# Kernel tuning notes

Measured on AMD Instinct MI355X. Metric: run time of the kernel, lower is better.

The kernel has to match this reference:

```python
import jax, jax.numpy as jnp
import numpy as np

B, C, W, H = 4, 256, 64, 64


def setup_inputs() -> dict:
    key = jax.random.key(0)
    ks = jax.random.split(key, 10)
    s = 1.0 / np.sqrt(C)  # fan-in style scale for 1x1 conv weights
    return {
        "x": jax.random.normal(ks[0], (B, C, W, H), dtype=jnp.float32),
        "Wq": jax.random.normal(ks[1], (C, C), dtype=jnp.float32) * s,
        "bq": jax.random.normal(ks[2], (C,), dtype=jnp.float32) * 0.02,
        "Wk": jax.random.normal(ks[3], (C, C), dtype=jnp.float32) * s,
        "bk": jax.random.normal(ks[4], (C,), dtype=jnp.float32) * 0.02,
        "Wv": jax.random.normal(ks[5], (C, C), dtype=jnp.float32) * s,
        "bv": jax.random.normal(ks[6], (C,), dtype=jnp.float32) * 0.02,
        "rel_h": jax.random.normal(ks[7], (1, C, H, 1), dtype=jnp.float32),
        "rel_w": jax.random.normal(ks[8], (1, C, 1, W), dtype=jnp.float32),
        # gamma is initialized to 0 in the original; use a nonzero value so the
        # attention branch actually contributes (otherwise out == x).
        "gamma": jnp.full((1,), 0.5, dtype=jnp.float32),
    }


def reference(x, Wq, bq, Wk, bk, Wv, bv, rel_h, rel_w, gamma):
    Bz, Cc, Ww, Hh = x.shape
    N = Ww * Hh
    xf = x.reshape(Bz, Cc, N)  # [B, C, N]

    # 1x1 convs == per-pixel linear projections over channels
    q = jnp.einsum('oc,bcn->bno', Wq, xf) + bq            # [B, N, C]
    k = jnp.einsum('oc,bcn->bon', Wk, xf) + bk[:, None]   # [B, C, N]
    v = jnp.einsum('oc,bcn->bon', Wv, xf) + bv[:, None]   # [B, C, N]

    # relative position bias: (rel_h + rel_w) -> [C, N], projected by q
    pos = (rel_h + rel_w).reshape(Cc, N)                  # [C, N]
    energy = jnp.einsum('bnc,bcm->bnm', q, k) + q @ pos   # [B, N, N]

    att = jax.nn.softmax(energy, axis=-1)                 # [B, N, N]

    # out[b,c,m] = sum_n v[b,c,n] * att[b,m,n]
    out = jnp.einsum('bcn,bmn->bcm', v, att).reshape(Bz, Cc, Ww, Hh)
    return gamma * out + x
```

## Files before the change

### kernel.cpp

```cpp
#include <hip/hip_runtime.h>
#include <stdint.h>

#define N_TOK 4096
#define C_DIM 256

typedef __attribute__((ext_vector_type(8))) short short8;
typedef __attribute__((ext_vector_type(8))) _Float16 half8;
typedef __attribute__((ext_vector_type(4))) float floatx4;
typedef __attribute__((ext_vector_type(4))) unsigned short ushort4v;

__device__ __forceinline__ unsigned short bf16_rne(float f) {
    union { float f; unsigned int u; } v; v.f = f;
    unsigned int u = v.u;
    unsigned int rounded = u + 0x7FFFu + ((u >> 16) & 1u);
    return (unsigned short)(rounded >> 16);
}
__device__ __forceinline__ float bf16_to_f(unsigned short h) {
    union { unsigned int u; float f; } v; v.u = ((unsigned int)h) << 16;
    return v.f;
}
__device__ __forceinline__ void split_bf16(float f, unsigned short& h, unsigned short& l) {
    h = bf16_rne(f);
    l = bf16_rne(f - bf16_to_f(h));
}
__device__ __forceinline__ unsigned short f2h(float f) {
    union { _Float16 h; unsigned short u; } v; v.h = (_Float16)f; return v.u;
}
__device__ __forceinline__ float h2f(unsigned short u) {
    union { unsigned short u; _Float16 h; } v; v.u = u; return (float)v.h;
}
__device__ __forceinline__ unsigned int pack2h(float a, float b) {
    union { _Float16 h[2]; unsigned int u; } v;
    v.h[0] = (_Float16)a; v.h[1] = (_Float16)b;
    return v.u;
}
__device__ __forceinline__ void g2l16(const void* g, void* l) {
    __builtin_amdgcn_global_load_lds(
        (const __attribute__((address_space(1))) void*)g,
        (__attribute__((address_space(3))) void*)l, 16, 0, 0);
}

__global__ __launch_bounds__(256) void prep_kernel(
    const float* __restrict__ x,
    const float* __restrict__ Wq, const float* __restrict__ Wk, const float* __restrict__ Wv,
    unsigned short* __restrict__ Xhi, unsigned short* __restrict__ Xlo,
    unsigned short* __restrict__ Whi, unsigned short* __restrict__ Wlo)
{
    const int t = threadIdx.x;
    if (blockIdx.x >= 1024) {
        const int pj = blockIdx.x - 1024;
        const float* W = (pj == 0) ? Wq : (pj == 1) ? Wk : Wv;
        unsigned short* dh = Whi + pj * 65536;
        unsigned short* dl = Wlo + pj * 65536;
        for (int it = 0; it < 64; it++) {
            const int idx = it * 1024 + t * 4;
            const float4 w = *(const float4*)&W[idx];
            unsigned short h0, l0, h1, l1, h2, l2, h3, l3;
            split_bf16(w.x, h0, l0); split_bf16(w.y, h1, l1);
            split_bf16(w.z, h2, l2); split_bf16(w.w, h3, l3);
            ushort4v vh; vh[0] = h0; vh[1] = h1; vh[2] = h2; vh[3] = h3;
            ushort4v vl; vl[0] = l0; vl[1] = l1; vl[2] = l2; vl[3] = l3;
            *(ushort4v*)&dh[idx] = vh;
            *(ushort4v*)&dl[idx] = vl;
        }
        return;
    }
    __shared__ float Xs[64 * 65];
    const int b  = blockIdx.x >> 8;
    const int ct = (blockIdx.x >> 6) & 3;
    const int nt = blockIdx.x & 63;
    const int c0 = ct * 64, n0 = nt * 64;
    {
        const int nch = t & 15, cr = t >> 4;
#pragma unroll
        for (int pass = 0; pass < 4; pass++) {
            const int c = pass * 16 + cr;
            const float4 v = *(const float4*)&x[((size_t)(b * C_DIM + c0 + c)) * N_TOK + n0 + nch * 4];
            float* row = &Xs[c * 65 + nch * 4];
            row[0] = v.x; row[1] = v.y; row[2] = v.z; row[3] = v.w;
        }
    }
    __syncthreads();
    {
        const int n = t >> 2, cc = t & 3;
        short8 vh0, vl0, vh1, vl1;
#pragma unroll
        for (int i = 0; i < 8; i++) {
            unsigned short h, l;
            split_bf16(Xs[(cc * 16 + i) * 65 + n], h, l);
            vh0[i] = (short)h; vl0[i] = (short)l;
        }
#pragma unroll
        for (int i = 0; i < 8; i++) {
            unsigned short h, l;
            split_bf16(Xs[(cc * 16 + 8 + i) * 65 + n], h, l);
            vh1[i] = (short)h; vl1[i] = (short)l;
        }
        const size_t off = ((size_t)b * N_TOK + n0 + n) * C_DIM + c0 + cc * 16;
        *(short8*)&Xhi[off] = vh0; *(short8*)&Xhi[off + 8] = vh1;
        *(short8*)&Xlo[off] = vl0; *(short8*)&Xlo[off + 8] = vl1;
    }
}

__global__ __launch_bounds__(256) void proj_kernel(
    const unsigned short* __restrict__ Xhi, const unsigned short* __restrict__ Xlo,
    const unsigned short* __restrict__ Whi, const unsigned short* __restrict__ Wlo,
    const float* __restrict__ bq, const float* __restrict__ bk, const float* __restrict__ bv,
    const float* __restrict__ relh, const float* __restrict__ relw,
    unsigned short* __restrict__ Qh,
    unsigned short* __restrict__ Kh,
    unsigned short* __restrict__ Vh)
{
    __shared__ unsigned short SM[20480];
    unsigned short* Ah = SM;
    unsigned short* Al = SM + 2048;
    unsigned short* Bh = SM + 4096;
    unsigned short* Bl = SM + 12288;

    const int t    = threadIdx.x;
    const int wave = t >> 6;
    const int lane = t & 63;
    const int l15  = lane & 15;
    const int quad = lane >> 4;

    const int bp   = blockIdx.x >> 6;
    const int proj = bp % 3;
    const int b    = bp / 3;
    const int n0   = (blockIdx.x & 63) * 64;

    const unsigned short* Xh = Xhi + ((size_t)b * N_TOK + n0) * C_DIM;
    const unsigned short* Xl = Xlo + ((size_t)b * N_TOK + n0) * C_DIM;
    const unsigned short* Wh = Whi + proj * 65536;
    const unsigned short* Wl = Wlo + proj * 65536;
    const float* bias = (proj == 0) ? bq : (proj == 1) ? bk : bv;
    const bool needlo = (proj < 2);

    floatx4 acc[16];
#pragma unroll
    for (int i = 0; i < 16; i++) acc[i] = (floatx4){0.f, 0.f, 0.f, 0.f};

    for (int c0 = 0; c0 < 256; c0 += 32) {
        {
            const int lr = lane >> 2, cp = lane & 3;
            const int key = (lr ^ (lr >> 2)) & 3;
            const int r = wave * 16 + lr;
            g2l16(Xh + (size_t)r * C_DIM + c0 + (cp ^ key) * 8, &Ah[wave * 512]);
            if (needlo) g2l16(Xl + (size_t)r * C_DIM + c0 + (cp ^ key) * 8, &Al[wave * 512]);
#pragma unroll
            for (int p = 0; p < 4; p++) {
                const int rb = (p * 4 + wave) * 16;
                const int rr = rb + lr;
                g2l16(Wh + (size_t)rr * 256 + c0 + (cp ^ key) * 8, &Bh[rb * 32]);
                if (needlo) g2l16(Wl + (size_t)rr * 256 + c0 + (cp ^ key) * 8, &Bl[rb * 32]);
            }
        }
        __syncthreads();

        const int akey = (l15 ^ (l15 >> 2)) & 3;
        const int arow = (wave * 16 + l15) * 32 + ((quad ^ akey) * 8);
        const short8 a_h = *(const short8*)&Ah[arow];
        short8 a_l;
        if (needlo) a_l = *(const short8*)&Al[arow];
#pragma unroll
        for (int ot = 0; ot < 16; ot++) {
            const int brow = (ot * 16 + l15) * 32 + ((quad ^ akey) * 8);
            const short8 b_h = *(const short8*)&Bh[brow];
            acc[ot] = __builtin_amdgcn_mfma_f32_16x16x32_bf16(a_h, b_h, acc[ot], 0, 0, 0);
            if (needlo) {
                const short8 b_l = *(const short8*)&Bl[brow];
                acc[ot] = __builtin_amdgcn_mfma_f32_16x16x32_bf16(a_l, b_h, acc[ot], 0, 0, 0);
                acc[ot] = __builtin_amdgcn_mfma_f32_16x16x32_bf16(a_h, b_l, acc[ot], 0, 0, 0);
            }
        }
        __syncthreads();
    }

    const int h0 = n0 >> 6;
    if (proj == 0) {
        unsigned short* Og = Qh + ((size_t)b * N_TOK + n0) * C_DIM;
#pragma unroll
        for (int ot = 0; ot < 16; ot++) {
            const int o = ot * 16 + l15;
            const float bs = bias[o];
#pragma unroll
            for (int r = 0; r < 4; r++) {
                const int nl = wave * 16 + quad * 4 + r;
                Og[(size_t)nl * C_DIM + o] = f2h(acc[ot][r] + bs);
            }
        }
    } else if (proj == 1) {
        unsigned short* Og = Kh + ((size_t)b * N_TOK + n0) * C_DIM;
#pragma unroll
        for (int ot = 0; ot < 16; ot++) {
            const int o = ot * 16 + l15;
            const float bs = bias[o];
            const float ph = relh[o * 64 + h0];
#pragma unroll
            for (int r = 0; r < 4; r++) {
                const int nl = wave * 16 + quad * 4 + r;
                Og[(size_t)nl * C_DIM + o] = f2h(acc[ot][r] + bs + ph + relw[o * 64 + nl]);
            }
        }
    } else {
        unsigned short* Vt = SM;
#pragma unroll
        for (int ot = 0; ot < 16; ot++) {
            const int o = ot * 16 + l15;
            const float bs = bias[o];
            const unsigned int u0 = (unsigned int)f2h(acc[ot][0] + bs) |
                                    ((unsigned int)f2h(acc[ot][1] + bs) << 16);
            const unsigned int u1 = (unsigned int)f2h(acc[ot][2] + bs) |
                                    ((unsigned int)f2h(acc[ot][3] + bs) << 16);
            uint2 uv; uv.x = u0; uv.y = u1;
            *(uint2*)&Vt[o * 72 + wave * 16 + quad * 4] = uv;
        }
        __syncthreads();
        const int ch   = t & 7;
        const int orow = t >> 3;
#pragma unroll
        for (int pass = 0; pass < 8; pass++) {
            const int o = pass * 32 + orow;
            const short8 vv = *(const short8*)&Vt[o * 72 + ch * 8];
            *(short8*)&Vh[((size_t)b * C_DIM + o) * N_TOK + n0 + ch * 8] = vv;
        }
    }
}

__global__ __launch_bounds__(256, 2) void flash_kernel(
    const unsigned short* __restrict__ Qg,
    const unsigned short* __restrict__ Kg,
    const unsigned short* __restrict__ Vg,
    unsigned short* __restrict__ Op,
    float* __restrict__ Lm)
{
    constexpr int NITER = 32;

    __shared__ unsigned short Ks[64 * 256];
    __shared__ unsigned short Vs[256 * 64];

    const int t    = threadIdx.x;
    const int wave = t >> 6;
    const int lane = t & 63;
    const int l15  = lane & 15;
    const int quad = lane >> 4;
    const int lk   = l15 & 7;

    const int bid = blockIdx.x;
    const int b   = bid & 3;
    const int s   = (bid >> 2) & 1;
    const int qt  = bid >> 3;

    const unsigned short* Kb = Kg + (size_t)b * N_TOK * C_DIM;
    const unsigned short* Vb = Vg + (size_t)b * C_DIM * N_TOK;

    half8 qf[8];
    const int qrow = qt * 64 + wave * 16 + l15;
    {
        const unsigned short* Qrow = Qg + ((size_t)b * N_TOK + qrow) * C_DIM;
#pragma unroll
        for (int ct = 0; ct < 8; ct++)
            qf[ct] = *(const half8*)&Qrow[ct * 32 + quad * 8];
    }

    floatx4 oacc[16];
#pragma unroll
    for (int i = 0; i < 16; i++) oacc[i] = (floatx4){0.f, 0.f, 0.f, 0.f};
    float m_i = -1e30f;
    float l_i = 0.f;

    const int jbase = s * (NITER * 64);
    const int oddq  = quad & 1;
    const int hiq   = quad >> 1;
    const int own   = (quad == 0) | (quad == 3);

    {
        const int lr = lane >> 5, cp = lane & 31;
#pragma unroll
        for (int p = 0; p < 8; p++) {
            const int jl = wave * 16 + p * 2 + lr;
            g2l16(Kb + (size_t)(jbase + jl) * C_DIM + (cp ^ (jl & 7)) * 8,
                  &Ks[(wave * 16 + p * 2) * 256]);
        }
    }

    for (int ti = 0; ti < NITER; ti++) {
        const int j0 = jbase + ti * 64;

        __syncthreads();

        {
            const int lr = lane >> 3, cp = lane & 7;
#pragma unroll
            for (int p = 0; p < 8; p++) {
                const int ob = (p * 4 + wave) * 8;
                const int o  = ob + lr;
                g2l16(Vb + (size_t)o * N_TOK + j0 + (cp ^ (o & 7)) * 8, &Vs[ob * 64]);
            }
        }

        floatx4 sv[4];
        __builtin_amdgcn_s_setprio(1);
#pragma unroll
        for (int jt = 0; jt < 4; jt++) {
            floatx4 a = (floatx4){0.f, 0.f, 0.f, 0.f};
#pragma unroll
            for (int ct = 0; ct < 8; ct++) {
                const half8 kb = *(const half8*)&Ks[(jt * 16 + l15) * 256 + (((ct * 4 + quad) ^ lk) * 8)];
                a = __builtin_amdgcn_mfma_f32_16x16x32_f16(kb, qf[ct], a, 0, 0, 0);
            }
            sv[jt] = a;
        }
        __builtin_amdgcn_s_setprio(0);

        float mx;
        {
            const float a0 = fmaxf(fmaxf(sv[0][0], sv[0][1]), fmaxf(sv[0][2], sv[0][3]));
            const float a1 = fmaxf(fmaxf(sv[1][0], sv[1][1]), fmaxf(sv[1][2], sv[1][3]));
            const float a2 = fmaxf(fmaxf(sv[2][0], sv[2][1]), fmaxf(sv[2][2], sv[2][3]));
            const float a3 = fmaxf(fmaxf(sv[3][0], sv[3][1]), fmaxf(sv[3][2], sv[3][3]));
            mx = fmaxf(fmaxf(a0, a1), fmaxf(a2, a3));
        }
        mx = fmaxf(mx, __shfl_xor(mx, 16));
        mx = fmaxf(mx, __shfl_xor(mx, 32));

        if (!__all(mx <= m_i + 8.f)) {
            const float mn    = fmaxf(m_i, mx);
            const float alpha = __expf(m_i - mn);
            m_i = mn;
            l_i *= alpha;
#pragma unroll
            for (int ot = 0; ot < 16; ot++) {
                oacc[ot][0] *= alpha; oacc[ot][1] *= alpha;
                oacc[ot][2] *= alpha; oacc[ot][3] *= alpha;
            }
        }
        float ps = 0.f;
#pragma unroll
        for (int jt = 0; jt < 4; jt++) {
#pragma unroll
            for (int r = 0; r < 4; r++) {
                const float p = __expf(sv[jt][r] - m_i);
                sv[jt][r] = p;
                ps += p;
            }
        }
        l_i += ps;

        half8 pf0, pf1;
        {
            const unsigned int u00 = pack2h(sv[0][0], sv[0][1]);
            const unsigned int u01 = pack2h(sv[0][2], sv[0][3]);
            const unsigned int u10 = pack2h(sv[1][0], sv[1][1]);
            const unsigned int u11 = pack2h(sv[1][2], sv[1][3]);
            const unsigned int t00 = __shfl_xor(u00, 16), t01 = __shfl_xor(u01, 16);
            const unsigned int t10 = __shfl_xor(u10, 16), t11 = __shfl_xor(u11, 16);
            const unsigned int L00 = oddq ? t00 : u00, H00 = oddq ? u00 : t00;
            const unsigned int L01 = oddq ? t01 : u01, H01 = oddq ? u01 : t01;
            const unsigned int L10 = oddq ? t10 : u10, H10 = oddq ? u10 : t10;
            const unsigned int L11 = oddq ? t11 : u11, H11 = oddq ? u11 : t11;
            const unsigned int ke0 = hiq ? L10 : L00, se0 = hiq ? L00 : L10;
            const unsigned int ke1 = hiq ? L11 : L01, se1 = hiq ? L01 : L11;
            const unsigned int ko0 = hiq ? H10 : H00, so0 = hiq ? H00 : H10;
            const unsigned int ko1 = hiq ? H11 : H01, so1 = hiq ? H01 : H11;
            const unsigned int re0 = __shfl_xor(se0, 32), re1 = __shfl_xor(se1, 32);
            const unsigned int ro0 = __shfl_xor(so0, 32), ro1 = __shfl_xor(so1, 32);
            union { unsigned int u[4]; half8 h; } pk;
            pk.u[0] = own ? ke0 : re0;
            pk.u[1] = own ? ke1 : re1;
            pk.u[2] = own ? ko0 : ro0;
            pk.u[3] = own ? ko1 : ro1;
            pf0 = pk.h;
        }
        {
            const unsigned int u00 = pack2h(sv[2][0], sv[2][1]);
            const unsigned int u01 = pack2h(sv[2][2], sv[2][3]);
            const unsigned int u10 = pack2h(sv[3][0], sv[3][1]);
            const unsigned int u11 = pack2h(sv[3][2], sv[3][3]);
            const unsigned int t00 = __shfl_xor(u00, 16), t01 = __shfl_xor(u01, 16);
            const unsigned int t10 = __shfl_xor(u10, 16), t11 = __shfl_xor(u11, 16);
            const unsigned int L00 = oddq ? t00 : u00, H00 = oddq ? u00 : t00;
            const unsigned int L01 = oddq ? t01 : u01, H01 = oddq ? u01 : t01;
            const unsigned int L10 = oddq ? t10 : u10, H10 = oddq ? u10 : t10;
            const unsigned int L11 = oddq ? t11 : u11, H11 = oddq ? u11 : t11;
            const unsigned int ke0 = hiq ? L10 : L00, se0 = hiq ? L00 : L10;
            const unsigned int ke1 = hiq ? L11 : L01, se1 = hiq ? L01 : L11;
            const unsigned int ko0 = hiq ? H10 : H00, so0 = hiq ? H00 : H10;
            const unsigned int ko1 = hiq ? H11 : H01, so1 = hiq ? H01 : H11;
            const unsigned int re0 = __shfl_xor(se0, 32), re1 = __shfl_xor(se1, 32);
            const unsigned int ro0 = __shfl_xor(so0, 32), ro1 = __shfl_xor(so1, 32);
            union { unsigned int u[4]; half8 h; } pk;
            pk.u[0] = own ? ke0 : re0;
            pk.u[1] = own ? ke1 : re1;
            pk.u[2] = own ? ko0 : ro0;
            pk.u[3] = own ? ko1 : ro1;
            pf1 = pk.h;
        }

        __syncthreads();

        if (ti < NITER - 1) {
            const int lr = lane >> 5, cp = lane & 31;
#pragma unroll
            for (int p = 0; p < 8; p++) {
                const int jl = wave * 16 + p * 2 + lr;
                g2l16(Kb + (size_t)(j0 + 64 + jl) * C_DIM + (cp ^ (jl & 7)) * 8,
                      &Ks[(wave * 16 + p * 2) * 256]);
            }
        }

        __builtin_amdgcn_s_setprio(1);
#pragma unroll
        for (int ot = 0; ot < 16; ot++) {
            const int row = (ot * 16 + l15) * 64;
            const half8 av0 = *(const half8*)&Vs[row + ((quad ^ lk) * 8)];
            const half8 av1 = *(const half8*)&Vs[row + (((4 + quad) ^ lk) * 8)];
            oacc[ot] = __builtin_amdgcn_mfma_f32_16x16x32_f16(av0, pf0, oacc[ot], 0, 0, 0);
            oacc[ot] = __builtin_amdgcn_mfma_f32_16x16x32_f16(av1, pf1, oacc[ot], 0, 0, 0);
        }
        __builtin_amdgcn_s_setprio(0);
    }

    unsigned short* Ob = Op + ((size_t)(s * 4 + b) * C_DIM) * N_TOK;
    const int n = qt * 64 + wave * 16 + l15;
#pragma unroll
    for (int ot = 0; ot < 16; ot++) {
#pragma unroll
        for (int r = 0; r < 4; r++) {
            const int c = ot * 16 + quad * 4 + r;
            Ob[(size_t)c * N_TOK + n] = f2h(oacc[ot][r]);
        }
    }
    float lt = l_i;
    lt += __shfl_xor(lt, 16);
    lt += __shfl_xor(lt, 32);
    if (quad == 0) {
        const size_t nb = (size_t)(s * 4 + b) * N_TOK + n;
        *(float2*)&Lm[nb * 2] = make_float2(m_i, lt);
    }
}

__global__ __launch_bounds__(256) void merge_kernel(
    const unsigned short* __restrict__ Op,
    const float* __restrict__ Lm,
    const float* __restrict__ x,
    const float* __restrict__ gamma,
    float* __restrict__ out)
{
    constexpr int NS = 2;
    const int blk = blockIdx.x;
    const int b   = blk >> 10;
    const int c   = (blk >> 2) & 255;
    const int nq  = blk & 3;
    const int n0  = nq * 1024 + threadIdx.x * 4;

    const size_t NEo = (size_t)4 * C_DIM * N_TOK;
    const size_t obase = ((size_t)b * C_DIM + c) * N_TOK + n0;

    float ms[NS][4], ls[NS][4], os[NS][4];
#pragma unroll
    for (int s = 0; s < NS; s++) {
        const uint2 u = *(const uint2*)&Op[s * NEo + obase];
        os[s][0] = h2f((unsigned short)(u.x & 0xffff));
        os[s][1] = h2f((unsigned short)(u.x >> 16));
        os[s][2] = h2f((unsigned short)(u.y & 0xffff));
        os[s][3] = h2f((unsigned short)(u.y >> 16));
        const float* Lms = Lm + (size_t)(s * 4 + b) * N_TOK * 2;
        const float4 A0 = *(const float4*)&Lms[n0 * 2];
        const float4 A1 = *(const float4*)&Lms[n0 * 2 + 4];
        ms[s][0] = A0.x; ls[s][0] = A0.y;
        ms[s][1] = A0.z; ls[s][1] = A0.w;
        ms[s][2] = A1.x; ls[s][2] = A1.y;
        ms[s][3] = A1.z; ls[s][3] = A1.w;
    }
    const float4 xv = *(const float4*)&x[obase];
    const float xin[4] = {xv.x, xv.y, xv.z, xv.w};
    const float g = gamma[0];

    float4 res;
    float* rp = (float*)&res;
#pragma unroll
    for (int i = 0; i < 4; i++) {
        float M = ms[0][i];
#pragma unroll
        for (int s = 1; s < NS; s++) M = fmaxf(M, ms[s][i]);
        float osum = 0.f, lsum = 0.f;
#pragma unroll
        for (int s = 0; s < NS; s++) {
            const float w = __expf(ms[s][i] - M);
            osum += w * os[s][i];
            lsum += w * ls[s][i];
        }
        rp[i] = g * osum / lsum + xin[i];
    }
    *(float4*)&out[obase] = res;
}

extern "C" void kernel_launch(void* const* d_in, const int* in_sizes, int n_in,
                              void* d_out, int out_size, void* d_ws, size_t ws_size,
                              hipStream_t stream) {
    const float* x     = (const float*)d_in[0];
    const float* Wq    = (const float*)d_in[1];
    const float* bq    = (const float*)d_in[2];
    const float* Wk    = (const float*)d_in[3];
    const float* bk    = (const float*)d_in[4];
    const float* Wv    = (const float*)d_in[5];
    const float* bv    = (const float*)d_in[6];
    const float* relh  = (const float*)d_in[7];
    const float* relw  = (const float*)d_in[8];
    const float* gamma = (const float*)d_in[9];
    float* out = (float*)d_out;

    const size_t NE = (size_t)4 * N_TOK * C_DIM;

    unsigned short* Op  = (unsigned short*)d_ws;
    unsigned short* Xhi = Op;
    unsigned short* Xlo = Op + NE;
    unsigned short* Whi = Op + (size_t)2 * NE;
    unsigned short* Wlo = Whi + 3 * 65536;
    unsigned short* Qh  = Wlo + 3 * 65536;
    unsigned short* Kh  = Qh + NE;
    unsigned short* Vh  = Kh + NE;
    float* Lm = (float*)(Vh + NE);

    hipLaunchKernelGGL(prep_kernel, dim3(1027), dim3(256), 0, stream,
                       x, Wq, Wk, Wv, Xhi, Xlo, Whi, Wlo);
    hipLaunchKernelGGL(proj_kernel, dim3(768), dim3(256), 0, stream,
                       Xhi, Xlo, Whi, Wlo, bq, bk, bv, relh, relw, Qh, Kh, Vh);
    hipLaunchKernelGGL(flash_kernel, dim3(512), dim3(256), 0, stream,
                       Qh, Kh, Vh, Op, Lm);
    hipLaunchKernelGGL(merge_kernel, dim3(4096), dim3(256), 0, stream,
                       Op, Lm, x, gamma, out);
}
```

Measured before the change: 249.6 us.

## Switch flash kernel to 32x32 MFMA tiles and 4-way KV split

Rewrites the attention kernel to use 32x32x16 MFMA instructions, so each wave owns 32 query rows instead of 16 and each block covers 128 queries. This cuts LDS fragment reads per FLOP and removes the complex cross-quad shuffle repacking of P. When the workspace is large enough, the KV range is split four ways (16 iterations per block) to keep 512 blocks in flight, and merge combines 4 partials. The cost is more accumulator registers (128 floats of oacc), which may pressure occupancy at 2 blocks/CU, plus extra partial-output traffic in the merge.

```diff
diff --git a/kernel.cpp b/kernel.cpp
--- a/kernel.cpp
+++ b/kernel.cpp
@@ -7,6 +7,7 @@
 typedef __attribute__((ext_vector_type(8))) short short8;
 typedef __attribute__((ext_vector_type(8))) _Float16 half8;
 typedef __attribute__((ext_vector_type(4))) float floatx4;
+typedef __attribute__((ext_vector_type(16))) float floatx16;
 typedef __attribute__((ext_vector_type(4))) unsigned short ushort4v;
 
 __device__ __forceinline__ unsigned short bf16_rne(float f) {
@@ -226,6 +227,7 @@
     }
 }
 
+template<int NITER>
 __global__ __launch_bounds__(256, 2) void flash_kernel(
     const unsigned short* __restrict__ Qg,
     const unsigned short* __restrict__ Kg,
@@ -233,7 +235,8 @@
     unsigned short* __restrict__ Op,
     float* __restrict__ Lm)
 {
-    constexpr int NITER = 32;
+    constexpr int NS  = N_TOK / (NITER * 64);
+    constexpr int QSH = (NS == 4) ? 4 : 3;
 
     __shared__ unsigned short Ks[64 * 256];
     __shared__ unsigned short Vs[256 * 64];
@@ -241,37 +244,36 @@
     const int t    = threadIdx.x;
     const int wave = t >> 6;
     const int lane = t & 63;
-    const int l15  = lane & 15;
-    const int quad = lane >> 4;
-    const int lk   = l15 & 7;
+    const int l31  = lane & 31;
+    const int H    = lane >> 5;
+    const int lk7  = lane & 7;
 
     const int bid = blockIdx.x;
     const int b   = bid & 3;
-    const int s   = (bid >> 2) & 1;
-    const int qt  = bid >> 3;
+    const int s   = (bid >> 2) & (NS - 1);
+    const int qt  = bid >> QSH;
 
     const unsigned short* Kb = Kg + (size_t)b * N_TOK * C_DIM;
     const unsigned short* Vb = Vg + (size_t)b * C_DIM * N_TOK;
 
-    half8 qf[8];
-    const int qrow = qt * 64 + wave * 16 + l15;
+    half8 qf[16];
+    const int q0 = qt * 128 + wave * 32;
     {
-        const unsigned short* Qrow = Qg + ((size_t)b * N_TOK + qrow) * C_DIM;
-#pragma unroll
-        for (int ct = 0; ct < 8; ct++)
-            qf[ct] = *(const half8*)&Qrow[ct * 32 + quad * 8];
-    }
-
-    floatx4 oacc[16];
-#pragma unroll
-    for (int i = 0; i < 16; i++) oacc[i] = (floatx4){0.f, 0.f, 0.f, 0.f};
+        const unsigned short* Qrow = Qg + ((size_t)b * N_TOK + q0 + l31) * C_DIM + H * 8;
+#pragma unroll
+        for (int ct = 0; ct < 16; ct++)
+            qf[ct] = *(const half8*)&Qrow[ct * 16];
+    }
+
+    floatx16 oacc[8];
+#pragma unroll
+    for (int cb = 0; cb < 8; cb++)
+#pragma unroll
+        for (int r = 0; r < 16; r++) oacc[cb][r] = 0.f;
     float m_i = -1e30f;
     float l_i = 0.f;
 
     const int jbase = s * (NITER * 64);
-    const int oddq  = quad & 1;
-    const int hiq   = quad >> 1;
-    const int own   = (quad == 0) | (quad == 3);
 
     {
         const int lr = lane >> 5, cp = lane & 31;
@@ -298,29 +300,31 @@
             }
         }
 
-        floatx4 sv[4];
-        __builtin_amdgcn_s_setprio(1);
-#pragma unroll
-        for (int jt = 0; jt < 4; jt++) {
-            floatx4 a = (floatx4){0.f, 0.f, 0.f, 0.f};
-#pragma unroll
-            for (int ct = 0; ct < 8; ct++) {
-                const half8 kb = *(const half8*)&Ks[(jt * 16 + l15) * 256 + (((ct * 4 + quad) ^ lk) * 8)];
-                a = __builtin_amdgcn_mfma_f32_16x16x32_f16(kb, qf[ct], a, 0, 0, 0);
-            }
-            sv[jt] = a;
-        }
-        __builtin_amdgcn_s_setprio(0);
-
-        float mx;
+        floatx16 sv0, sv1;
         {
-            const float a0 = fmaxf(fmaxf(sv[0][0], sv[0][1]), fmaxf(sv[0][2], sv[0][3]));
-            const float a1 = fmaxf(fmaxf(sv[1][0], sv[1][1]), fmaxf(sv[1][2], sv[1][3]));
-            const float a2 = fmaxf(fmaxf(sv[2][0], sv[2][1]), fmaxf(sv[2][2], sv[2][3]));
-            const float a3 = fmaxf(fmaxf(sv[3][0], sv[3][1]), fmaxf(sv[3][2], sv[3][3]));
-            mx = fmaxf(fmaxf(a0, a1), fmaxf(a2, a3));
-        }
-        mx = fmaxf(mx, __shfl_xor(mx, 16));
+            floatx16 a0, a1;
+#pragma unroll
+            for (int r = 0; r < 16; r++) { a0[r] = 0.f; a1[r] = 0.f; }
+            const int rb0 = l31 * 256;
+            const int rb1 = (32 + l31) * 256;
+            __builtin_amdgcn_s_setprio(1);
+#pragma unroll
+            for (int ct = 0; ct < 16; ct++) {
+                const int ch = ((ct * 2 + H) ^ lk7) * 8;
+                const half8 k0 = *(const half8*)&Ks[rb0 + ch];
+                a0 = __builtin_amdgcn_mfma_f32_32x32x16_f16(k0, qf[ct], a0, 0, 0, 0);
+                const half8 k1 = *(const half8*)&Ks[rb1 + ch];
+                a1 = __builtin_amdgcn_mfma_f32_32x32x16_f16(k1, qf[ct], a1, 0, 0, 0);
+            }
+            __builtin_amdgcn_s_setprio(0);
+            sv0 = a0; sv1 = a1;
+        }
+
+        float mx = sv0[0];
+#pragma unroll
+        for (int r = 1; r < 16; r++) mx = fmaxf(mx, sv0[r]);
+#pragma unroll
+        for (int r = 0; r < 16; r++) mx = fmaxf(mx, sv1[r]);
         mx = fmaxf(mx, __shfl_xor(mx, 32));
 
         if (!__all(mx <= m_i + 8.f)) {
@@ -329,71 +333,71 @@
             m_i = mn;
             l_i *= alpha;
 #pragma unroll
-            for (int ot = 0; ot < 16; ot++) {
-                oacc[ot][0] *= alpha; oacc[ot][1] *= alpha;
-                oacc[ot][2] *= alpha; oacc[ot][3] *= alpha;
-            }
+            for (int cb = 0; cb < 8; cb++)
+#pragma unroll
+                for (int r = 0; r < 16; r++) oacc[cb][r] *= alpha;
         }
         float ps = 0.f;
 #pragma unroll
-        for (int jt = 0; jt < 4; jt++) {
-#pragma unroll
-            for (int r = 0; r < 4; r++) {
-                const float p = __expf(sv[jt][r] - m_i);
-                sv[jt][r] = p;
-                ps += p;
-            }
+        for (int r = 0; r < 16; r++) {
+            const float p = __expf(sv0[r] - m_i);
+            sv0[r] = p; ps += p;
+        }
+#pragma unroll
+        for (int r = 0; r < 16; r++) {
+            const float p = __expf(sv1[r] - m_i);
+            sv1[r] = p; ps += p;
         }
         l_i += ps;
 
-        half8 pf0, pf1;
+        half8 pf0, pf1, pf2, pf3;
         {
-            const unsigned int u00 = pack2h(sv[0][0], sv[0][1]);
-            const unsigned int u01 = pack2h(sv[0][2], sv[0][3]);
-            const unsigned int u10 = pack2h(sv[1][0], sv[1][1]);
-            const unsigned int u11 = pack2h(sv[1][2], sv[1][3]);
-            const unsigned int t00 = __shfl_xor(u00, 16), t01 = __shfl_xor(u01, 16);
-            const unsigned int t10 = __shfl_xor(u10, 16), t11 = __shfl_xor(u11, 16);
-            const unsigned int L00 = oddq ? t00 : u00, H00 = oddq ? u00 : t00;
-            const unsigned int L01 = oddq ? t01 : u01, H01 = oddq ? u01 : t01;
-            const unsigned int L10 = oddq ? t10 : u10, H10 = oddq ? u10 : t10;
-            const unsigned int L11 = oddq ? t11 : u11, H11 = oddq ? u11 : t11;
-            const unsigned int ke0 = hiq ? L10 : L00, se0 = hiq ? L00 : L10;
-            const unsigned int ke1 = hiq ? L11 : L01, se1 = hiq ? L01 : L11;
-            const unsigned int ko0 = hiq ? H10 : H00, so0 = hiq ? H00 : H10;
-            const unsigned int ko1 = hiq ? H11 : H01, so1 = hiq ? H01 : H11;
-            const unsigned int re0 = __shfl_xor(se0, 32), re1 = __shfl_xor(se1, 32);
-            const unsigned int ro0 = __shfl_xor(so0, 32), ro1 = __shfl_xor(so1, 32);
-            union { unsigned int u[4]; half8 h; } pk;
-            pk.u[0] = own ? ke0 : re0;
-            pk.u[1] = own ? ke1 : re1;
-            pk.u[2] = own ? ko0 : ro0;
-            pk.u[3] = own ? ko1 : ro1;
-            pf0 = pk.h;
+            const unsigned int p0 = pack2h(sv0[0],  sv0[1]);
+            const unsigned int p1 = pack2h(sv0[2],  sv0[3]);
+            const unsigned int p2 = pack2h(sv0[4],  sv0[5]);
+            const unsigned int p3 = pack2h(sv0[6],  sv0[7]);
+            const unsigned int p4 = pack2h(sv0[8],  sv0[9]);
+            const unsigned int p5 = pack2h(sv0[10], sv0[11]);
+            const unsigned int p6 = pack2h(sv0[12], sv0[13]);
+            const unsigned int p7 = pack2h(sv0[14], sv0[15]);
+            const unsigned int s0 = __shfl_xor(p0, 32);
+            const unsigned int s1 = __shfl_xor(p1, 32);
+            const unsigned int s2 = __shfl_xor(p2, 32);
+            const unsigned int s3 = __shfl_xor(p3, 32);
+            const unsigned int s4 = __shfl_xor(p4, 32);
+            const unsigned int s5 = __shfl_xor(p5, 32);
+            const unsigned int s6 = __shfl_xor(p6, 32);
+            const unsigned int s7 = __shfl_xor(p7, 32);
+            union { unsigned int u[4]; half8 h; } a, c;
+            a.u[0] = H ? s2 : p0;  a.u[1] = H ? s3 : p1;
+            a.u[2] = H ? p2 : s0;  a.u[3] = H ? p3 : s1;
+            c.u[0] = H ? s6 : p4;  c.u[1] = H ? s7 : p5;
+            c.u[2] = H ? p6 : s4;  c.u[3] = H ? p7 : s5;
+            pf0 = a.h; pf1 = c.h;
         }
         {
-            const unsigned int u00 = pack2h(sv[2][0], sv[2][1]);
-            const unsigned int u01 = pack2h(sv[2][2], sv[2][3]);
-            const unsigned int u10 = pack2h(sv[3][0], sv[3][1]);
-            const unsigned int u11 = pack2h(sv[3][2], sv[3][3]);
-            const unsigned int t00 = __shfl_xor(u00, 16), t01 = __shfl_xor(u01, 16);
-            const unsigned int t10 = __shfl_xor(u10, 16), t11 = __shfl_xor(u11, 16);
-            const unsigned int L00 = oddq ? t00 : u00, H00 = oddq ? u00 : t00;
-            const unsigned int L01 = oddq ? t01 : u01, H01 = oddq ? u01 : t01;
-            const unsigned int L10 = oddq ? t10 : u10, H10 = oddq ? u10 : t10;
-            const unsigned int L11 = oddq ? t11 : u11, H11 = oddq ? u11 : t11;
-            const unsigned int ke0 = hiq ? L10 : L00, se0 = hiq ? L00 : L10;
-            const unsigned int ke1 = hiq ? L11 : L01, se1 = hiq ? L01 : L11;
-            const unsigned int ko0 = hiq ? H10 : H00, so0 = hiq ? H00 : H10;
-            const unsigned int ko1 = hiq ? H11 : H01, so1 = hiq ? H01 : H11;
-            const unsigned int re0 = __shfl_xor(se0, 32), re1 = __shfl_xor(se1, 32);
-            const unsigned int ro0 = __shfl_xor(so0, 32), ro1 = __shfl_xor(so1, 32);
-            union { unsigned int u[4]; half8 h; } pk;
-            pk.u[0] = own ? ke0 : re0;
-            pk.u[1] = own ? ke1 : re1;
-            pk.u[2] = own ? ko0 : ro0;
-            pk.u[3] = own ? ko1 : ro1;
-            pf1 = pk.h;
+            const unsigned int p0 = pack2h(sv1[0],  sv1[1]);
+            const unsigned int p1 = pack2h(sv1[2],  sv1[3]);
+            const unsigned int p2 = pack2h(sv1[4],  sv1[5]);
+            const unsigned int p3 = pack2h(sv1[6],  sv1[7]);
+            const unsigned int p4 = pack2h(sv1[8],  sv1[9]);
+            const unsigned int p5 = pack2h(sv1[10], sv1[11]);
+            const unsigned int p6 = pack2h(sv1[12], sv1[13]);
+            const unsigned int p7 = pack2h(sv1[14], sv1[15]);
+            const unsigned int s0 = __shfl_xor(p0, 32);
+            const unsigned int s1 = __shfl_xor(p1, 32);
+            const unsigned int s2 = __shfl_xor(p2, 32);
+            const unsigned int s3 = __shfl_xor(p3, 32);
+            const unsigned int s4 = __shfl_xor(p4, 32);
+            const unsigned int s5 = __shfl_xor(p5, 32);
+            const unsigned int s6 = __shfl_xor(p6, 32);
+            const unsigned int s7 = __shfl_xor(p7, 32);
+            union { unsigned int u[4]; half8 h; } a, c;
+            a.u[0] = H ? s2 : p0;  a.u[1] = H ? s3 : p1;
+            a.u[2] = H ? p2 : s0;  a.u[3] = H ? p3 : s1;
+            c.u[0] = H ? s6 : p4;  c.u[1] = H ? s7 : p5;
+            c.u[2] = H ? p6 : s4;  c.u[3] = H ? p7 : s5;
+            pf2 = a.h; pf3 = c.h;
         }
 
         __syncthreads();
@@ -410,35 +414,38 @@
 
         __builtin_amdgcn_s_setprio(1);
 #pragma unroll
-        for (int ot = 0; ot < 16; ot++) {
-            const int row = (ot * 16 + l15) * 64;
-            const half8 av0 = *(const half8*)&Vs[row + ((quad ^ lk) * 8)];
-            const half8 av1 = *(const half8*)&Vs[row + (((4 + quad) ^ lk) * 8)];
-            oacc[ot] = __builtin_amdgcn_mfma_f32_16x16x32_f16(av0, pf0, oacc[ot], 0, 0, 0);
-            oacc[ot] = __builtin_amdgcn_mfma_f32_16x16x32_f16(av1, pf1, oacc[ot], 0, 0, 0);
+        for (int cb = 0; cb < 8; cb++) {
+            const int vb = (cb * 32 + l31) * 64;
+            const half8 av0 = *(const half8*)&Vs[vb + (((0 + H) ^ lk7) * 8)];
+            oacc[cb] = __builtin_amdgcn_mfma_f32_32x32x16_f16(av0, pf0, oacc[cb], 0, 0, 0);
+            const half8 av1 = *(const half8*)&Vs[vb + (((2 + H) ^ lk7) * 8)];
+            oacc[cb] = __builtin_amdgcn_mfma_f32_32x32x16_f16(av1, pf1, oacc[cb], 0, 0, 0);
+            const half8 av2 = *(const half8*)&Vs[vb + (((4 + H) ^ lk7) * 8)];
+            oacc[cb] = __builtin_amdgcn_mfma_f32_32x32x16_f16(av2, pf2, oacc[cb], 0, 0, 0);
+            const half8 av3 = *(const half8*)&Vs[vb + (((6 + H) ^ lk7) * 8)];
+            oacc[cb] = __builtin_amdgcn_mfma_f32_32x32x16_f16(av3, pf3, oacc[cb], 0, 0, 0);
         }
         __builtin_amdgcn_s_setprio(0);
     }
 
     unsigned short* Ob = Op + ((size_t)(s * 4 + b) * C_DIM) * N_TOK;
-    const int n = qt * 64 + wave * 16 + l15;
-#pragma unroll
-    for (int ot = 0; ot < 16; ot++) {
-#pragma unroll
-        for (int r = 0; r < 4; r++) {
-            const int c = ot * 16 + quad * 4 + r;
-            Ob[(size_t)c * N_TOK + n] = f2h(oacc[ot][r]);
-        }
-    }
-    float lt = l_i;
-    lt += __shfl_xor(lt, 16);
-    lt += __shfl_xor(lt, 32);
-    if (quad == 0) {
+    const int n = q0 + l31;
+#pragma unroll
+    for (int cb = 0; cb < 8; cb++) {
+#pragma unroll
+        for (int r = 0; r < 16; r++) {
+            const int c = cb * 32 + (r & 3) + 8 * (r >> 2) + 4 * H;
+            Ob[(size_t)c * N_TOK + n] = f2h(oacc[cb][r]);
+        }
+    }
+    float lt = l_i + __shfl_xor(l_i, 32);
+    if (H == 0) {
         const size_t nb = (size_t)(s * 4 + b) * N_TOK + n;
         *(float2*)&Lm[nb * 2] = make_float2(m_i, lt);
     }
 }
 
+template<int NS>
 __global__ __launch_bounds__(256) void merge_kernel(
     const unsigned short* __restrict__ Op,
     const float* __restrict__ Lm,
@@ -446,7 +453,6 @@
     const float* __restrict__ gamma,
     float* __restrict__ out)
 {
-    constexpr int NS = 2;
     const int blk = blockIdx.x;
     const int b   = blk >> 10;
     const int c   = (blk >> 2) & 255;
@@ -512,10 +518,13 @@
 
     const size_t NE = (size_t)4 * N_TOK * C_DIM;
 
+    const size_t need4 = ((size_t)7 * NE + 6 * 65536) * 2 + (size_t)4 * 4 * N_TOK * 2 * 4;
+    const int NS = (ws_size >= need4) ? 4 : 2;
+
     unsigned short* Op  = (unsigned short*)d_ws;
     unsigned short* Xhi = Op;
     unsigned short* Xlo = Op + NE;
-    unsigned short* Whi = Op + (size_t)2 * NE;
+    unsigned short* Whi = Op + (size_t)NS * NE;
     unsigned short* Wlo = Whi + 3 * 65536;
     unsigned short* Qh  = Wlo + 3 * 65536;
     unsigned short* Kh  = Qh + NE;
@@ -526,8 +535,15 @@
                        x, Wq, Wk, Wv, Xhi, Xlo, Whi, Wlo);
     hipLaunchKernelGGL(proj_kernel, dim3(768), dim3(256), 0, stream,
                        Xhi, Xlo, Whi, Wlo, bq, bk, bv, relh, relw, Qh, Kh, Vh);
-    hipLaunchKernelGGL(flash_kernel, dim3(512), dim3(256), 0, stream,
-                       Qh, Kh, Vh, Op, Lm);
-    hipLaunchKernelGGL(merge_kernel, dim3(4096), dim3(256), 0, stream,
-                       Op, Lm, x, gamma, out);
-}
+    if (NS == 4) {
+        hipLaunchKernelGGL((flash_kernel<16>), dim3(512), dim3(256), 0, stream,
+                           Qh, Kh, Vh, Op, Lm);
+        hipLaunchKernelGGL((merge_kernel<4>), dim3(4096), dim3(256), 0, stream,
+                           Op, Lm, x, gamma, out);
+    } else {
+        hipLaunchKernelGGL((flash_kernel<32>), dim3(256), dim3(256), 0, stream,
+                           Qh, Kh, Vh, Op, Lm);
+        hipLaunchKernelGGL((merge_kernel<2>), dim3(4096), dim3(256), 0, stream,
+                           Op, Lm, x, gamma, out);
+    }
+}
```

After: 463.5 us. 85.7% more time.
